# Performance work log

Hardware: AMD Instinct MI355X
Metric: run time of the kernel (lower is better)

## Reference

```python
import jax, jax.numpy as jnp
import numpy as np

B, N = 8192, 512
WEIGHT_THRESHOLD = 0.0
EPS = 1e-5


def setup_inputs() -> dict:
    key = jax.random.key(0)
    k1, k2, k3 = jax.random.split(key, 3)
    src_points = jax.random.normal(k1, (B, N, 3), dtype=jnp.float32)
    tgt_points = jax.random.normal(k2, (B, N, 3), dtype=jnp.float32)
    weights = jax.random.uniform(k3, (B, N), dtype=jnp.float32)
    return {"src_points": src_points, "tgt_points": tgt_points, "weights": weights}


def _weighted_procrustes(src, tgt, w):
    # threshold + normalize weights  (B, N)
    w = jnp.where(w < WEIGHT_THRESHOLD, jnp.zeros_like(w), w)
    w = w / (jnp.sum(w, axis=1, keepdims=True) + EPS)
    w3 = w[..., None]                                   # (B, N, 1)
    # weighted centroids (B, 1, 3)
    src_c = jnp.sum(w3 * src, axis=1, keepdims=True)
    tgt_c = jnp.sum(w3 * tgt, axis=1, keepdims=True)
    src0 = src - src_c
    tgt0 = tgt - tgt_c
    # weighted covariance H = src0^T (w * tgt0)  -> (B, 3, 3)
    H = jnp.einsum("bni,bnj->bij", src0, w3 * tgt0)
    U, S, Vh = jnp.linalg.svd(H)
    V = jnp.swapaxes(Vh, -1, -2)
    Ut = jnp.swapaxes(U, -1, -2)
    # reflection correction: diag(1, 1, sign(det(V U^T)))
    det = jnp.linalg.det(jnp.matmul(V, Ut))             # (B,)
    ones = jnp.ones((src.shape[0], 2), dtype=src.dtype)
    d = jnp.concatenate([ones, jnp.sign(det)[:, None]], axis=1)  # (B, 3)
    R = jnp.einsum("bij,bj,bjk->bik", V, d, Ut)         # (B, 3, 3)
    t = tgt_c[:, 0, :] - jnp.einsum("bij,bj->bi", R, src_c[:, 0, :])  # (B, 3)
    return R, t


def reference(src_points, tgt_points, weights):
    return _weighted_procrustes(src_points, tgt_points, weights)
```

## Files before the change

kernel.cpp:

```cpp
#include <hip/hip_runtime.h>

#define NPTS 512
#define BLOCK 256

__global__ __launch_bounds__(BLOCK) void wproc_moments(
    const float* __restrict__ src,
    const float* __restrict__ tgt,
    const float* __restrict__ wts,
    float* __restrict__ ws)
{
    const int b = blockIdx.x;
    const int t = threadIdx.x;

    __shared__ float s_s[NPTS * 3];
    __shared__ float s_t[NPTS * 3];
    __shared__ float s_w[NPTS];

    {
        const float4* sb4 = (const float4*)(src + (size_t)b * (NPTS * 3));
        const float4* tb4 = (const float4*)(tgt + (size_t)b * (NPTS * 3));
        const float4* wb4 = (const float4*)(wts + (size_t)b * NPTS);
        float4* ss4 = (float4*)s_s;
        float4* st4 = (float4*)s_t;
        float4* sw4 = (float4*)s_w;
        const int n4 = NPTS * 3 / 4;
        for (int i = t; i < n4; i += BLOCK) { ss4[i] = sb4[i]; st4[i] = tb4[i]; }
        if (t < NPTS / 4) sw4[t] = wb4[t];
    }
    __syncthreads();

    float acc[16];
    #pragma unroll
    for (int i = 0; i < 16; ++i) acc[i] = 0.f;

    #pragma unroll
    for (int k = 0; k < NPTS / BLOCK; ++k) {
        const int p = t + k * BLOCK;
        float w = s_w[p];
        w = (w < 0.f) ? 0.f : w;
        const float sx = s_s[3 * p + 0], sy = s_s[3 * p + 1], sz = s_s[3 * p + 2];
        const float tx = s_t[3 * p + 0], ty = s_t[3 * p + 1], tz = s_t[3 * p + 2];
        acc[0] += w;
        acc[1] += w * sx; acc[2] += w * sy; acc[3] += w * sz;
        acc[4] += w * tx; acc[5] += w * ty; acc[6] += w * tz;
        const float wsx = w * sx, wsy = w * sy, wsz = w * sz;
        acc[7]  += wsx * tx; acc[8]  += wsx * ty; acc[9]  += wsx * tz;
        acc[10] += wsy * tx; acc[11] += wsy * ty; acc[12] += wsy * tz;
        acc[13] += wsz * tx; acc[14] += wsz * ty; acc[15] += wsz * tz;
    }

    #pragma unroll
    for (int off = 32; off > 0; off >>= 1) {
        #pragma unroll
        for (int i = 0; i < 16; ++i)
            acc[i] += __shfl_down(acc[i], off, 64);
    }

    __shared__ float red[BLOCK / 64][16];
    const int wave = t >> 6, lane = t & 63;
    if (lane == 0) {
        #pragma unroll
        for (int i = 0; i < 16; ++i) red[wave][i] = acc[i];
    }
    __syncthreads();

    if (t < 16) {
        ws[(size_t)b * 16 + t] =
            red[0][t] + red[1][t] + red[2][t] + red[3][t];
    }
}

__global__ __launch_bounds__(BLOCK) void wproc_solve(
    const float* __restrict__ ws,
    float* __restrict__ out,
    int B)
{
    const int b = blockIdx.x * BLOCK + threadIdx.x;
    if (b >= B) return;

    double m[16];
    #pragma unroll
    for (int i = 0; i < 16; ++i) m[i] = (double)ws[(size_t)b * 16 + i];

    const double T = m[0] + 1e-5;
    const double f = 2.0 - m[0] / T;
    const double cs[3] = { m[1] / T, m[2] / T, m[3] / T };
    const double ct[3] = { m[4] / T, m[5] / T, m[6] / T };
    double H[3][3];
    for (int i = 0; i < 3; ++i)
        for (int j = 0; j < 3; ++j)
            H[i][j] = m[7 + i * 3 + j] / T - f * cs[i] * ct[j];

    double A[3][3];
    for (int i = 0; i < 3; ++i)
        for (int j = 0; j < 3; ++j)
            A[i][j] = H[0][i] * H[0][j] + H[1][i] * H[1][j] + H[2][i] * H[2][j];

    double V[3][3] = { {1, 0, 0}, {0, 1, 0}, {0, 0, 1} };
    for (int sweep = 0; sweep < 8; ++sweep) {
        for (int pair = 0; pair < 3; ++pair) {
            const int p = (pair == 2) ? 1 : 0;
            const int q = (pair == 0) ? 1 : 2;
            const double apq = A[p][q];
            if (fabs(apq) < 1e-40) continue;
            const double theta = (A[q][q] - A[p][p]) / (2.0 * apq);
            const double tt = ((theta >= 0.0) ? 1.0 : -1.0)
                            / (fabs(theta) + sqrt(theta * theta + 1.0));
            const double c = 1.0 / sqrt(tt * tt + 1.0);
            const double sn = tt * c;
            for (int k = 0; k < 3; ++k) {
                const double akp = A[k][p], akq = A[k][q];
                A[k][p] = c * akp - sn * akq;
                A[k][q] = sn * akp + c * akq;
            }
            for (int k = 0; k < 3; ++k) {
                const double apk = A[p][k], aqk = A[q][k];
                A[p][k] = c * apk - sn * aqk;
                A[q][k] = sn * apk + c * aqk;
            }
            for (int k = 0; k < 3; ++k) {
                const double vkp = V[k][p], vkq = V[k][q];
                V[k][p] = c * vkp - sn * vkq;
                V[k][q] = sn * vkp + c * vkq;
            }
        }
    }

    const double lam[3] = { A[0][0], A[1][1], A[2][2] };
    int i0 = 0, i1 = 1, i2 = 2;
    if (lam[i0] < lam[i1]) { int tmp = i0; i0 = i1; i1 = tmp; }
    if (lam[i0] < lam[i2]) { int tmp = i0; i0 = i2; i2 = tmp; }
    if (lam[i1] < lam[i2]) { int tmp = i1; i1 = i2; i2 = tmp; }

    const double v1[3] = { V[0][i0], V[1][i0], V[2][i0] };
    const double v2[3] = { V[0][i1], V[1][i1], V[2][i1] };
    const double v3[3] = { v1[1] * v2[2] - v1[2] * v2[1],
                           v1[2] * v2[0] - v1[0] * v2[2],
                           v1[0] * v2[1] - v1[1] * v2[0] };

    double u1[3], u2[3], u3[3];
    for (int i = 0; i < 3; ++i)
        u1[i] = H[i][0] * v1[0] + H[i][1] * v1[1] + H[i][2] * v1[2];
    double n1 = sqrt(u1[0] * u1[0] + u1[1] * u1[1] + u1[2] * u1[2]);
    n1 = (n1 > 1e-30) ? n1 : 1e-30;
    for (int i = 0; i < 3; ++i) u1[i] /= n1;

    for (int i = 0; i < 3; ++i)
        u2[i] = H[i][0] * v2[0] + H[i][1] * v2[1] + H[i][2] * v2[2];
    const double d12 = u1[0] * u2[0] + u1[1] * u2[1] + u1[2] * u2[2];
    for (int i = 0; i < 3; ++i) u2[i] -= d12 * u1[i];
    double n2 = sqrt(u2[0] * u2[0] + u2[1] * u2[1] + u2[2] * u2[2]);
    n2 = (n2 > 1e-30) ? n2 : 1e-30;
    for (int i = 0; i < 3; ++i) u2[i] /= n2;

    u3[0] = u1[1] * u2[2] - u1[2] * u2[1];
    u3[1] = u1[2] * u2[0] - u1[0] * u2[2];
    u3[2] = u1[0] * u2[1] - u1[1] * u2[0];

    double R[3][3];
    for (int i = 0; i < 3; ++i)
        for (int j = 0; j < 3; ++j)
            R[i][j] = v1[i] * u1[j] + v2[i] * u2[j] + v3[i] * u3[j];

    double tv[3];
    for (int i = 0; i < 3; ++i)
        tv[i] = ct[i] - (R[i][0] * cs[0] + R[i][1] * cs[1] + R[i][2] * cs[2]);

    float* outR = out + (size_t)b * 9;
    for (int i = 0; i < 3; ++i)
        for (int j = 0; j < 3; ++j)
            outR[i * 3 + j] = (float)R[i][j];
    float* outT = out + (size_t)B * 9 + (size_t)b * 3;
    for (int i = 0; i < 3; ++i) outT[i] = (float)tv[i];
}

extern "C" void kernel_launch(void* const* d_in, const int* in_sizes, int n_in,
                              void* d_out, int out_size, void* d_ws, size_t ws_size,
                              hipStream_t stream) {
    const float* src = (const float*)d_in[0];
    const float* tgt = (const float*)d_in[1];
    const float* wts = (const float*)d_in[2];
    float* out = (float*)d_out;
    float* ws = (float*)d_ws;
    const int B = out_size / 12;

    wproc_moments<<<B, BLOCK, 0, stream>>>(src, tgt, wts, ws);
    wproc_solve<<<(B + BLOCK - 1) / BLOCK, BLOCK, 0, stream>>>(ws, out, B);
}
```

Before: 160.3 us.

## Map one batch per wavefront with register-resident loads and LDS transpose reduction

The moments kernel now assigns each batch element to a single 64-lane wavefront instead of a 256-thread block. Each lane loads 8 consecutive points directly into registers with float4 loads, which removes the LDS staging copy. The per-wave shuffle reduction is replaced by an LDS transpose followed by a 16-lane row sum. The Jacobi eigen-solver also drops from 8 to 5 sweeps, with an exact-zero skip test, which trades some convergence margin for fewer double-precision operations. The grid is sized B/4 and assumes B is divisible by 4.

```diff
diff --git a/kernel.cpp b/kernel.cpp
--- a/kernel.cpp
+++ b/kernel.cpp
@@ -2,6 +2,7 @@
 
 #define NPTS 512
 #define BLOCK 256
+#define WAVES_PER_BLOCK 4
 
 __global__ __launch_bounds__(BLOCK) void wproc_moments(
     const float* __restrict__ src,
@@ -9,37 +10,41 @@
     const float* __restrict__ wts,
     float* __restrict__ ws)
 {
-    const int b = blockIdx.x;
-    const int t = threadIdx.x;
+    const int wave = threadIdx.x >> 6;
+    const int lane = threadIdx.x & 63;
+    const int b = blockIdx.x * WAVES_PER_BLOCK + wave;
 
-    __shared__ float s_s[NPTS * 3];
-    __shared__ float s_t[NPTS * 3];
-    __shared__ float s_w[NPTS];
+    const float4* s4 = (const float4*)(src + (size_t)b * (NPTS * 3)) + 6 * lane;
+    const float4* t4 = (const float4*)(tgt + (size_t)b * (NPTS * 3)) + 6 * lane;
+    const float4* w4 = (const float4*)(wts + (size_t)b * NPTS) + 2 * lane;
 
-    {
-        const float4* sb4 = (const float4*)(src + (size_t)b * (NPTS * 3));
-        const float4* tb4 = (const float4*)(tgt + (size_t)b * (NPTS * 3));
-        const float4* wb4 = (const float4*)(wts + (size_t)b * NPTS);
-        float4* ss4 = (float4*)s_s;
-        float4* st4 = (float4*)s_t;
-        float4* sw4 = (float4*)s_w;
-        const int n4 = NPTS * 3 / 4;
-        for (int i = t; i < n4; i += BLOCK) { ss4[i] = sb4[i]; st4[i] = tb4[i]; }
-        if (t < NPTS / 4) sw4[t] = wb4[t];
+    float4 sv[6], tv[6], wv[2];
+    #pragma unroll
+    for (int k = 0; k < 6; ++k) { sv[k] = s4[k]; tv[k] = t4[k]; }
+    wv[0] = w4[0];
+    wv[1] = w4[1];
+
+    float sf[24], tf[24], wf[8];
+    #pragma unroll
+    for (int k = 0; k < 6; ++k) {
+        sf[4 * k + 0] = sv[k].x; sf[4 * k + 1] = sv[k].y;
+        sf[4 * k + 2] = sv[k].z; sf[4 * k + 3] = sv[k].w;
+        tf[4 * k + 0] = tv[k].x; tf[4 * k + 1] = tv[k].y;
+        tf[4 * k + 2] = tv[k].z; tf[4 * k + 3] = tv[k].w;
     }
-    __syncthreads();
+    wf[0] = wv[0].x; wf[1] = wv[0].y; wf[2] = wv[0].z; wf[3] = wv[0].w;
+    wf[4] = wv[1].x; wf[5] = wv[1].y; wf[6] = wv[1].z; wf[7] = wv[1].w;
 
     float acc[16];
     #pragma unroll
     for (int i = 0; i < 16; ++i) acc[i] = 0.f;
 
     #pragma unroll
-    for (int k = 0; k < NPTS / BLOCK; ++k) {
-        const int p = t + k * BLOCK;
-        float w = s_w[p];
+    for (int j = 0; j < 8; ++j) {
+        float w = wf[j];
         w = (w < 0.f) ? 0.f : w;
-        const float sx = s_s[3 * p + 0], sy = s_s[3 * p + 1], sz = s_s[3 * p + 2];
-        const float tx = s_t[3 * p + 0], ty = s_t[3 * p + 1], tz = s_t[3 * p + 2];
+        const float sx = sf[3 * j + 0], sy = sf[3 * j + 1], sz = sf[3 * j + 2];
+        const float tx = tf[3 * j + 0], ty = tf[3 * j + 1], tz = tf[3 * j + 2];
         acc[0] += w;
         acc[1] += w * sx; acc[2] += w * sy; acc[3] += w * sz;
         acc[4] += w * tx; acc[5] += w * ty; acc[6] += w * tz;
@@ -49,24 +54,20 @@
         acc[13] += wsz * tx; acc[14] += wsz * ty; acc[15] += wsz * tz;
     }
 
+    __shared__ float xp[WAVES_PER_BLOCK][16][68];
     #pragma unroll
-    for (int off = 32; off > 0; off >>= 1) {
-        #pragma unroll
-        for (int i = 0; i < 16; ++i)
-            acc[i] += __shfl_down(acc[i], off, 64);
-    }
-
-    __shared__ float red[BLOCK / 64][16];
-    const int wave = t >> 6, lane = t & 63;
-    if (lane == 0) {
-        #pragma unroll
-        for (int i = 0; i < 16; ++i) red[wave][i] = acc[i];
-    }
+    for (int m = 0; m < 16; ++m) xp[wave][m][lane] = acc[m];
     __syncthreads();
 
-    if (t < 16) {
-        ws[(size_t)b * 16 + t] =
-            red[0][t] + red[1][t] + red[2][t] + red[3][t];
+    if (lane < 16) {
+        const float4* row = (const float4*)&xp[wave][lane][0];
+        float4 s = row[0];
+        #pragma unroll
+        for (int k = 1; k < 16; ++k) {
+            float4 r = row[k];
+            s.x += r.x; s.y += r.y; s.z += r.z; s.w += r.w;
+        }
+        ws[(size_t)b * 16 + lane] = (s.x + s.y) + (s.z + s.w);
     }
 }
 
@@ -97,12 +98,12 @@
             A[i][j] = H[0][i] * H[0][j] + H[1][i] * H[1][j] + H[2][i] * H[2][j];
 
     double V[3][3] = { {1, 0, 0}, {0, 1, 0}, {0, 0, 1} };
-    for (int sweep = 0; sweep < 8; ++sweep) {
+    for (int sweep = 0; sweep < 5; ++sweep) {
         for (int pair = 0; pair < 3; ++pair) {
             const int p = (pair == 2) ? 1 : 0;
             const int q = (pair == 0) ? 1 : 2;
             const double apq = A[p][q];
-            if (fabs(apq) < 1e-40) continue;
+            if (apq == 0.0) continue;
             const double theta = (A[q][q] - A[p][p]) / (2.0 * apq);
             const double tt = ((theta >= 0.0) ? 1.0 : -1.0)
                             / (fabs(theta) + sqrt(theta * theta + 1.0));
@@ -184,6 +185,6 @@
     float* ws = (float*)d_ws;
     const int B = out_size / 12;
 
-    wproc_moments<<<B, BLOCK, 0, stream>>>(src, tgt, wts, ws);
+    wproc_moments<<<B / WAVES_PER_BLOCK, BLOCK, 0, stream>>>(src, tgt, wts, ws);
     wproc_solve<<<(B + BLOCK - 1) / BLOCK, BLOCK, 0, stream>>>(ws, out, B);
 }
```

Measured after the change: 149.0 us. 7.0% less time.
